# Kernel tuning notes

Measured on AMD Instinct MI355X. Metric: run time of the kernel, lower is better.

Reference implementation:

```python
import jax, jax.numpy as jnp
import numpy as np
import math

B, S, D, NH, HFF, E, K, C, L, V = 8, 256, 1024, 16, 2048, 8, 2, 10, 4, 32000
HD = D // NH
EPS = 1e-5


def _pos_encoding(max_len, d_model):
    pos = jnp.arange(max_len, dtype=jnp.float32)[:, None]
    div = jnp.exp(jnp.arange(0, d_model, 2, dtype=jnp.float32) * (-math.log(10000.0) / d_model))
    pe = jnp.zeros((max_len, d_model), dtype=jnp.float32)
    pe = pe.at[:, 0::2].set(jnp.sin(pos * div))
    pe = pe.at[:, 1::2].set(jnp.cos(pos * div))
    return pe[:, None, :]  # [max_len, 1, D], matching torch buffer layout


def _layernorm(x, g, b):
    mu = jnp.mean(x, axis=-1, keepdims=True)
    var = jnp.mean((x - mu) ** 2, axis=-1, keepdims=True)
    return (x - mu) * jax.lax.rsqrt(var + EPS) * g + b


def setup_inputs() -> dict:
    key = jax.random.key(0)
    ks = jax.random.split(key, 20)
    sc = lambda *shape: 0.02
    inp = {
        "src": jax.random.randint(ks[0], (B, S), 0, V, dtype=jnp.int32),
        "emb": jax.random.normal(ks[1], (V, D), jnp.float32) * 0.02,
        "in_proj_w": jax.random.normal(ks[2], (L, 3 * D, D), jnp.float32) * 0.02,
        "in_proj_b": jnp.zeros((L, 3 * D), jnp.float32),
        "out_w": jax.random.normal(ks[3], (L, D, D), jnp.float32) * 0.02,
        "out_b": jnp.zeros((L, D), jnp.float32),
        "ln1_g": jnp.ones((L, D), jnp.float32),
        "ln1_b": jnp.zeros((L, D), jnp.float32),
        "ln2_g": jnp.ones((L, D), jnp.float32),
        "ln2_b": jnp.zeros((L, D), jnp.float32),
        "gate_w": jax.random.normal(ks[4], (L, E, D), jnp.float32) * 0.02,
        "gate_b": jnp.zeros((L, E), jnp.float32),
        "w1": jax.random.normal(ks[5], (L, E, D, HFF), jnp.float32) * 0.02,
        "b1": jnp.zeros((L, E, HFF), jnp.float32),
        "w2": jax.random.normal(ks[6], (L, E, HFF, D), jnp.float32) * 0.02,
        "b2": jnp.zeros((L, E, D), jnp.float32),
        "cls_w": jax.random.normal(ks[7], (C, D), jnp.float32) * 0.02,
        "cls_b": jnp.zeros((C,), jnp.float32),
    }
    return inp


def _attention(x, ipw, ipb, ow, ob):
    # x: [B,S,D]
    qkv = x @ ipw.T + ipb  # [B,S,3D]
    q, k, v = jnp.split(qkv, 3, axis=-1)
    q = q.reshape(B, S, NH, HD)
    k = k.reshape(B, S, NH, HD)
    v = v.reshape(B, S, NH, HD)
    scores = jnp.einsum("bqhd,bkhd->bhqk", q, k) / math.sqrt(HD)
    attn = jax.nn.softmax(scores, axis=-1)
    o = jnp.einsum("bhqk,bkhd->bqhd", attn, v).reshape(B, S, D)
    return o @ ow.T + ob


def _moe(x, gw, gb, w1, b1, w2, b2):
    # x: [B,S,D]; gw: [E,D]; w1: [E,D,H]; w2: [E,H,D]
    t = x.reshape(B * S, D)
    logits = t @ gw.T + gb  # [T,E]
    topv, topi = jax.lax.top_k(logits, K)  # [T,K]
    weights = jax.nn.softmax(topv, axis=-1)  # [T,K]
    # dense expert compute (small E, compute-bound), combine via top-k gather
    h = jax.nn.relu(jnp.einsum("td,edh->teh", t, w1) + b1)  # [T,E,H]
    y = jnp.einsum("teh,ehd->ted", h, w2) + b2  # [T,E,D]
    sel = jnp.take_along_axis(y, topi[:, :, None], axis=1)  # [T,K,D]
    out = jnp.sum(sel * weights[:, :, None], axis=1)  # [T,D]
    return out.reshape(B, S, D), logits.reshape(B, S, E)


def reference(src, emb, in_proj_w, in_proj_b, out_w, out_b, ln1_g, ln1_b,
              ln2_g, ln2_b, gate_w, gate_b, w1, b1, w2, b2, cls_w, cls_b):
    x = emb[src] * math.sqrt(D)  # [B,S,D]
    pe = _pos_encoding(5000, D)  # [max_len,1,D]
    # faithful to original: pe indexed by batch dim (x.size(0)), broadcast over seq
    x = x + pe[:B]  # [B,1,D] -> broadcast [B,S,D]
    all_gates = []
    for l in range(in_proj_w.shape[0]):
        a = _attention(x, in_proj_w[l], in_proj_b[l], out_w[l], out_b[l])
        x = _layernorm(x + a, ln1_g[l], ln1_b[l])
        m, g = _moe(x, gate_w[l], gate_b[l], w1[l], b1[l], w2[l], b2[l])
        x = _layernorm(x + m, ln2_g[l], ln2_b[l])
        all_gates.append(g)
    pooled = jnp.mean(x, axis=1)  # [B,D]
    out = pooled @ cls_w.T + cls_b  # [B,C]
    return out, jnp.stack(all_gates)  # ([B,C], [L,B,S,E])
```

## Files before the change

### kernel.cpp

```cpp
#include <hip/hip_runtime.h>
#include <math.h>

#define TKN 2048
#define DIM 1024
#define NHEAD 16
#define HDIM 64
#define HFF 2048
#define NE 8
#define TOPK 2
#define NCLS 10
#define NLAYER 4
#define SEQ 256
#define BATCH 8

typedef __attribute__((ext_vector_type(8))) _Float16 f16x8;
typedef __attribute__((ext_vector_type(4))) float f32x4;

__device__ __forceinline__ unsigned short f2h(float v) {
  _Float16 h = (_Float16)v;
  return __builtin_bit_cast(unsigned short, h);
}
__device__ __forceinline__ float h2f(unsigned short u) {
  return (float)__builtin_bit_cast(_Float16, u);
}
__device__ __forceinline__ void fsplit(float v, unsigned short& hi, unsigned short& lo) {
  _Float16 h = (_Float16)v;
  hi = __builtin_bit_cast(unsigned short, h);
  lo = f2h(v - (float)h);
}

__device__ __forceinline__ void gload_lds16(const void* g, void* l) {
  __builtin_amdgcn_global_load_lds((__attribute__((address_space(1))) void*)g,
                                   (__attribute__((address_space(3))) void*)l,
                                   16, 0, 0);
}

__global__ __launch_bounds__(256) void k_embed(const int* __restrict__ src,
                                               const float* __restrict__ emb,
                                               float* __restrict__ x,
                                               unsigned short* __restrict__ xhi,
                                               unsigned short* __restrict__ xlo) {
  const int t = blockIdx.x;
  const int tid = threadIdx.x;
  const int b = t / SEQ;
  const int tok = src[t];
  const float* erow = emb + (size_t)tok * DIM;
  const size_t base = (size_t)t * DIM;
  const float cexp = -9.210340371976184f / 1024.0f;
#pragma unroll
  for (int j = 0; j < 4; ++j) {
    int d = tid + 256 * j;
    int i2 = d & ~1;
    float ang = (float)b * expf((float)i2 * cexp);
    float pe = (d & 1) ? cosf(ang) : sinf(ang);
    float v = erow[d] * 32.0f + pe;
    x[base + d] = v;
    fsplit(v, xhi[base + d], xlo[base + d]);
  }
}

__global__ __launch_bounds__(256) void k_cvt_split(const float* __restrict__ in,
                                                   unsigned short* __restrict__ ohi,
                                                   unsigned short* __restrict__ olo) {
  int i = blockIdx.x * 256 + threadIdx.x;
  float4 v = ((const float4*)in)[i];
  ushort4 h, l;
  fsplit(v.x, h.x, l.x); fsplit(v.y, h.y, l.y);
  fsplit(v.z, h.z, l.z); fsplit(v.w, h.w, l.w);
  ((ushort4*)ohi)[i] = h;
  ((ushort4*)olo)[i] = l;
}

__global__ __launch_bounds__(256) void k_cvt_t_split(const float* __restrict__ in,
                                                     unsigned short* __restrict__ ohi,
                                                     unsigned short* __restrict__ olo,
                                                     int R, int Cc) {
  __shared__ float t[32][33];
  const int tx = threadIdx.x & 31, ty = threadIdx.x >> 5;
  const int c0 = blockIdx.x * 32, r0 = blockIdx.y * 32;
  const float* ip = in + (size_t)blockIdx.z * R * Cc;
  const size_t obase = (size_t)blockIdx.z * R * Cc;
#pragma unroll
  for (int j = 0; j < 4; ++j)
    t[ty + 8 * j][tx] = ip[(size_t)(r0 + ty + 8 * j) * Cc + c0 + tx];
  __syncthreads();
#pragma unroll
  for (int j = 0; j < 4; ++j) {
    unsigned short hi, lo;
    fsplit(t[tx][ty + 8 * j], hi, lo);
    size_t o = obase + (size_t)(c0 + ty + 8 * j) * R + r0 + tx;
    ohi[o] = hi;
    olo[o] = lo;
  }
}

template <int MODE, bool RELU, int OUTK, bool SPLIT>
__global__ __launch_bounds__(256) void k_mfma_gemm(
    const unsigned short* __restrict__ Ahi, const unsigned short* __restrict__ Alo,
    const unsigned short* __restrict__ Bhi, const unsigned short* __restrict__ Blo,
    const float* __restrict__ bias, void* __restrict__ out0, void* __restrict__ out1,
    int M, int N, int K,
    const int* __restrict__ slot_token, const int* __restrict__ offg) {
  __shared__ unsigned short U[SPLIT ? 2 : 1][128 * 64];
  const int tid = threadIdx.x;
  const int w = tid >> 6, lane = tid & 63;
  const int bm = blockIdx.y * 128, bn = blockIdx.x * 128;
  int r0 = 0, rows = M, e = 0;
  if (MODE != 0) {
    e = blockIdx.z;
    r0 = offg[e];
    rows = offg[e + 1] - r0;
    if (bm >= rows) return;
  }
  const size_t bwb = (size_t)e * K * N;
  const float* biasq = bias + (size_t)e * N;

  const int lrow8 = lane >> 3;
  const int s = (lane & 7) ^ lrow8;
  const int chunk = (s & 3) * 8;
  const unsigned short* sp0[4];
  const unsigned short* sp1[4];
#pragma unroll
  for (int i = 0; i < 4; ++i) {
    int rloc = w * 32 + i * 8 + lrow8;
    int growA;
    if (MODE == 0) {
      growA = bm + rloc;
    } else {
      int rr = bm + rloc;
      if (rr >= rows) rr = rows - 1;
      growA = (MODE == 1) ? slot_token[r0 + rr] : (r0 + rr);
    }
    size_t aoff = (size_t)growA * K + chunk;
    size_t boff = bwb + (size_t)(bn + rloc) * K + chunk;
    if constexpr (SPLIT) {
      sp0[i] = (s < 4 ? Ahi : Alo) + aoff;
      sp1[i] = (s < 4 ? Bhi : Blo) + boff;
    } else {
      sp0[i] = (s < 4) ? (Ahi + aoff) : (Bhi + boff);
      sp1[i] = nullptr;
    }
  }

  f32x4 acc[4][4] = {};
  const int wr = w >> 1, wc = w & 1;
  const int lr = lane & 15, lg = lane >> 4;
  const int sw = lr & 7;
  unsigned aoffs[4], boffs[4];
#pragma unroll
  for (int m = 0; m < 4; ++m)
    aoffs[m] = (unsigned)((wr * 64 + m * 16 + lr) * 64 + ((lg ^ sw) * 8));
#pragma unroll
  for (int n = 0; n < 4; ++n)
    boffs[n] = (unsigned)((wc * 64 + n * 16 + lr) * 64 + ((lg ^ sw) * 8));

  for (int k0 = 0; k0 < K; k0 += 32) {
#pragma unroll
    for (int i = 0; i < 4; ++i) {
      gload_lds16(sp0[i], &U[0][(w * 32 + i * 8) * 64]);
      sp0[i] += 32;
      if constexpr (SPLIT) {
        gload_lds16(sp1[i], &U[1][(w * 32 + i * 8) * 64]);
        sp1[i] += 32;
      }
    }
    __syncthreads();
    f16x8 afh[4], bfh[4], afl[4], bfl[4];
    if constexpr (SPLIT) {
#pragma unroll
      for (int m = 0; m < 4; ++m) afh[m] = *(const f16x8*)&U[0][aoffs[m]];
#pragma unroll
      for (int m = 0; m < 4; ++m) afl[m] = *(const f16x8*)&U[0][aoffs[m] ^ 32];
#pragma unroll
      for (int n = 0; n < 4; ++n) bfh[n] = *(const f16x8*)&U[1][boffs[n]];
#pragma unroll
      for (int n = 0; n < 4; ++n) bfl[n] = *(const f16x8*)&U[1][boffs[n] ^ 32];
    } else {
#pragma unroll
      for (int m = 0; m < 4; ++m) afh[m] = *(const f16x8*)&U[0][aoffs[m]];
#pragma unroll
      for (int n = 0; n < 4; ++n) bfh[n] = *(const f16x8*)&U[0][boffs[n] ^ 32];
    }
#pragma unroll
    for (int m = 0; m < 4; ++m)
#pragma unroll
      for (int n = 0; n < 4; ++n) {
        acc[m][n] = __builtin_amdgcn_mfma_f32_16x16x32_f16(afh[m], bfh[n], acc[m][n], 0, 0, 0);
        if constexpr (SPLIT) {
          acc[m][n] = __builtin_amdgcn_mfma_f32_16x16x32_f16(afh[m], bfl[n], acc[m][n], 0, 0, 0);
          acc[m][n] = __builtin_amdgcn_mfma_f32_16x16x32_f16(afl[m], bfh[n], acc[m][n], 0, 0, 0);
        }
      }
    __syncthreads();
  }

  float bv[4];
#pragma unroll
  for (int n = 0; n < 4; ++n) bv[n] = biasq[bn + wc * 64 + n * 16 + lr];

#pragma unroll
  for (int m = 0; m < 4; ++m) {
#pragma unroll
    for (int j = 0; j < 4; ++j) {
      int rowg = bm + wr * 64 + m * 16 + lg * 4 + j;
      if (MODE != 0 && rowg >= rows) continue;
      size_t crow = (size_t)((MODE == 0) ? rowg : (r0 + rowg)) * N;
#pragma unroll
      for (int n = 0; n < 4; ++n) {
        float v = acc[m][n][j] + bv[n];
        if (RELU) v = fmaxf(v, 0.f);
        size_t o = crow + bn + wc * 64 + n * 16 + lr;
        if (OUTK == 0) {
          ((float*)out0)[o] = v;
        } else if (OUTK == 1) {
          ((unsigned short*)out0)[o] = f2h(v);
        } else {
          unsigned short hi, lo;
          fsplit(v, hi, lo);
          ((unsigned short*)out0)[o] = hi;
          ((unsigned short*)out1)[o] = lo;
        }
      }
    }
  }
}

__global__ __launch_bounds__(256) void k_attn(const float* __restrict__ qkv,
                                              unsigned short* __restrict__ ohi,
                                              unsigned short* __restrict__ olo) {
  const int qt = blockIdx.x;
  const int hh = blockIdx.y;
  const int bb = blockIdx.z;
  const int tid = threadIdx.x;
  __shared__ float qs[16][64];
  __shared__ float ps[16][256];
  const int t0 = bb * SEQ + qt * 16;
  for (int i = tid; i < 16 * 64; i += 256) {
    int qi = i >> 6, d = i & 63;
    qs[qi][d] = qkv[(size_t)(t0 + qi) * (3 * DIM) + hh * 64 + d];
  }
  __syncthreads();
  float s[16];
#pragma unroll
  for (int qi = 0; qi < 16; ++qi) s[qi] = 0.f;
  const float* krow = qkv + (size_t)(bb * SEQ + tid) * (3 * DIM) + DIM + hh * 64;
#pragma unroll 4
  for (int c = 0; c < 16; ++c) {
    float4 kv = *(const float4*)(krow + c * 4);
#pragma unroll
    for (int qi = 0; qi < 16; ++qi) {
      s[qi] += kv.x * qs[qi][c * 4 + 0] + kv.y * qs[qi][c * 4 + 1] +
               kv.z * qs[qi][c * 4 + 2] + kv.w * qs[qi][c * 4 + 3];
    }
  }
#pragma unroll
  for (int qi = 0; qi < 16; ++qi) ps[qi][tid] = s[qi] * 0.125f;
  __syncthreads();
  const int wv = tid >> 6, lane = tid & 63;
  for (int rr = wv; rr < 16; rr += 4) {
    float v[4];
#pragma unroll
    for (int j = 0; j < 4; ++j) v[j] = ps[rr][lane + 64 * j];
    float m = fmaxf(fmaxf(v[0], v[1]), fmaxf(v[2], v[3]));
    for (int msk = 32; msk; msk >>= 1) m = fmaxf(m, __shfl_xor(m, msk));
    float e[4], sum = 0.f;
#pragma unroll
    for (int j = 0; j < 4; ++j) { e[j] = expf(v[j] - m); sum += e[j]; }
    for (int msk = 32; msk; msk >>= 1) sum += __shfl_xor(sum, msk);
    float inv = 1.0f / sum;
#pragma unroll
    for (int j = 0; j < 4; ++j) ps[rr][lane + 64 * j] = e[j] * inv;
  }
  __syncthreads();
  const int qi0 = tid >> 6, d = tid & 63;
  float acc[4] = {0.f, 0.f, 0.f, 0.f};
  const float* vbase = qkv + (size_t)(bb * SEQ) * (3 * DIM) + 2 * DIM + hh * 64 + d;
  for (int k = 0; k < 256; ++k) {
    float vv = vbase[(size_t)k * (3 * DIM)];
    acc[0] += ps[qi0][k] * vv;
    acc[1] += ps[qi0 + 4][k] * vv;
    acc[2] += ps[qi0 + 8][k] * vv;
    acc[3] += ps[qi0 + 12][k] * vv;
  }
#pragma unroll
  for (int j = 0; j < 4; ++j) {
    size_t o = (size_t)(t0 + qi0 + 4 * j) * DIM + hh * 64 + d;
    fsplit(acc[j], ohi[o], olo[o]);
  }
}

__device__ __forceinline__ float block_reduce_sum(float v, float* red) {
  const int tid = threadIdx.x;
  red[tid] = v;
  __syncthreads();
  for (int s = 128; s > 0; s >>= 1) {
    if (tid < s) red[tid] += red[tid + s];
    __syncthreads();
  }
  float r = red[0];
  __syncthreads();
  return r;
}

__global__ __launch_bounds__(256) void k_add_ln(const float* __restrict__ xin,
                                                const float* __restrict__ add,
                                                const float* __restrict__ g,
                                                const float* __restrict__ bt,
                                                float* __restrict__ xout,
                                                unsigned short* __restrict__ xhi,
                                                unsigned short* __restrict__ xlo) {
  __shared__ float red[256];
  const int t = blockIdx.x, tid = threadIdx.x;
  const size_t base = (size_t)t * DIM;
  float v[4];
  float s = 0.f;
#pragma unroll
  for (int j = 0; j < 4; ++j) {
    int d = tid + 256 * j;
    v[j] = xin[base + d] + add[base + d];
    s += v[j];
  }
  float mean = block_reduce_sum(s, red) * (1.0f / DIM);
  float s2 = 0.f;
#pragma unroll
  for (int j = 0; j < 4; ++j) { float dv = v[j] - mean; s2 += dv * dv; }
  float var = block_reduce_sum(s2, red) * (1.0f / DIM);
  float rs = rsqrtf(var + 1e-5f);
#pragma unroll
  for (int j = 0; j < 4; ++j) {
    int d = tid + 256 * j;
    float o = (v[j] - mean) * rs * g[d] + bt[d];
    xout[base + d] = o;
    fsplit(o, xhi[base + d], xlo[base + d]);
  }
}

__global__ __launch_bounds__(256) void k_gate(const float* __restrict__ x,
                                              const float* __restrict__ gw,
                                              const float* __restrict__ gb,
                                              float* __restrict__ gout,
                                              int* __restrict__ topi,
                                              float* __restrict__ topw) {
  __shared__ float xs[DIM];
  __shared__ float lgs[NE];
  const int t = blockIdx.x, tid = threadIdx.x;
#pragma unroll
  for (int j = 0; j < 4; ++j) xs[tid + 256 * j] = x[(size_t)t * DIM + tid + 256 * j];
  __syncthreads();
  const int eg = tid >> 5, l32 = tid & 31;
  const float* wrow = gw + (size_t)eg * DIM;
  float p = 0.f;
  for (int j = 0; j < 32; ++j) {
    int d = l32 + 32 * j;
    p += xs[d] * wrow[d];
  }
  for (int m = 16; m; m >>= 1) p += __shfl_xor(p, m);
  if (l32 == 0) lgs[eg] = p;
  __syncthreads();
  if (tid < NE) {
    float v = lgs[tid] + gb[tid];
    gout[(size_t)t * NE + tid] = v;
    lgs[tid] = v;
  }
  __syncthreads();
  if (tid == 0) {
    int i0 = 0; float v0 = lgs[0];
    for (int i = 1; i < NE; ++i) if (lgs[i] > v0) { v0 = lgs[i]; i0 = i; }
    int i1 = -1; float v1 = -1e30f;
    for (int i = 0; i < NE; ++i) { if (i == i0) continue; if (lgs[i] > v1) { v1 = lgs[i]; i1 = i; } }
    float e1 = expf(v1 - v0);
    float w0 = 1.0f / (1.0f + e1);
    topi[2 * t] = i0; topi[2 * t + 1] = i1;
    topw[2 * t] = w0; topw[2 * t + 1] = e1 * w0;
  }
}

__global__ __launch_bounds__(512) void k_route(const int* __restrict__ topi,
                                               int* __restrict__ offg,
                                               int* __restrict__ slot_token,
                                               int* __restrict__ slot_of) {
  __shared__ int cnt_s[NE];
  __shared__ int off_s[NE + 1];
  const int tid = threadIdx.x;
  const int w = tid >> 6, lane = tid & 63;
  int c = 0;
  for (int i = lane; i < TKN * TOPK; i += 64) c += (topi[i] == w) ? 1 : 0;
  for (int m = 32; m; m >>= 1) c += __shfl_xor(c, m);
  if (lane == 0) cnt_s[w] = c;
  __syncthreads();
  if (tid == 0) {
    off_s[0] = 0;
    for (int e2 = 0; e2 < NE; ++e2) off_s[e2 + 1] = off_s[e2] + cnt_s[e2];
    for (int e2 = 0; e2 <= NE; ++e2) offg[e2] = off_s[e2];
  }
  __syncthreads();
  int base = off_s[w];
  for (int i0 = 0; i0 < TKN * TOPK; i0 += 64) {
    int i = i0 + lane;
    bool mm = (topi[i] == w);
    unsigned long long mask = __ballot(mm ? 1 : 0);
    int rank = __popcll(mask & ((1ull << lane) - 1ull));
    if (mm) {
      int slot = base + rank;
      slot_token[slot] = i >> 1;
      slot_of[i] = slot;
    }
    base += __popcll(mask);
  }
}

__global__ __launch_bounds__(256) void k_moe_combine_ln(const float* __restrict__ xin,
                                                        const float* __restrict__ y,
                                                        const float* __restrict__ topw,
                                                        const int* __restrict__ slot_of,
                                                        const float* __restrict__ g,
                                                        const float* __restrict__ bt,
                                                        float* __restrict__ xout,
                                                        unsigned short* __restrict__ xhi,
                                                        unsigned short* __restrict__ xlo) {
  __shared__ float red[256];
  const int t = blockIdx.x, tid = threadIdx.x;
  const float w0 = topw[2 * t], w1v = topw[2 * t + 1];
  const int s0 = slot_of[2 * t], s1 = slot_of[2 * t + 1];
  const size_t base = (size_t)t * DIM;
  float v[4];
  float s = 0.f;
#pragma unroll
  for (int j = 0; j < 4; ++j) {
    int d = tid + 256 * j;
    v[j] = xin[base + d] + w0 * y[(size_t)s0 * DIM + d] + w1v * y[(size_t)s1 * DIM + d];
    s += v[j];
  }
  float mean = block_reduce_sum(s, red) * (1.0f / DIM);
  float s2 = 0.f;
#pragma unroll
  for (int j = 0; j < 4; ++j) { float dv = v[j] - mean; s2 += dv * dv; }
  float var = block_reduce_sum(s2, red) * (1.0f / DIM);
  float rs = rsqrtf(var + 1e-5f);
#pragma unroll
  for (int j = 0; j < 4; ++j) {
    int d = tid + 256 * j;
    float o = (v[j] - mean) * rs * g[d] + bt[d];
    xout[base + d] = o;
    fsplit(o, xhi[base + d], xlo[base + d]);
  }
}

__global__ __launch_bounds__(256) void k_pool_cls(const float* __restrict__ x,
                                                  const float* __restrict__ cw,
                                                  const float* __restrict__ cb,
                                                  float* __restrict__ out) {
  __shared__ float pooled[DIM];
  const int b = blockIdx.x, tid = threadIdx.x;
  float a[4] = {0.f, 0.f, 0.f, 0.f};
  for (int s = 0; s < SEQ; ++s) {
    const float* row = x + (size_t)(b * SEQ + s) * DIM;
#pragma unroll
    for (int j = 0; j < 4; ++j) a[j] += row[tid + 256 * j];
  }
#pragma unroll
  for (int j = 0; j < 4; ++j) pooled[tid + 256 * j] = a[j] * (1.0f / SEQ);
  __syncthreads();
  const int wv = tid >> 6, lane = tid & 63;
  for (int c = wv; c < NCLS; c += 4) {
    float p = 0.f;
    for (int d = lane; d < DIM; d += 64) p += pooled[d] * cw[(size_t)c * DIM + d];
    for (int m = 32; m; m >>= 1) p += __shfl_xor(p, m);
    if (lane == 0) out[b * NCLS + c] = p + cb[c];
  }
}

extern "C" void kernel_launch(void* const* d_in, const int* in_sizes, int n_in,
                              void* d_out, int out_size, void* d_ws, size_t ws_size,
                              hipStream_t stream) {
  const int*   src  = (const int*)  d_in[0];
  const float* emb  = (const float*)d_in[1];
  const float* ipw  = (const float*)d_in[2];
  const float* ipb  = (const float*)d_in[3];
  const float* ow   = (const float*)d_in[4];
  const float* ob   = (const float*)d_in[5];
  const float* ln1g = (const float*)d_in[6];
  const float* ln1b = (const float*)d_in[7];
  const float* ln2g = (const float*)d_in[8];
  const float* ln2b = (const float*)d_in[9];
  const float* gw   = (const float*)d_in[10];
  const float* gb   = (const float*)d_in[11];
  const float* w1   = (const float*)d_in[12];
  const float* b1   = (const float*)d_in[13];
  const float* w2   = (const float*)d_in[14];
  const float* b2   = (const float*)d_in[15];
  const float* cw   = (const float*)d_in[16];
  const float* cb   = (const float*)d_in[17];
  float* out = (float*)d_out;

  char* ws = (char*)d_ws;
  size_t off = 0;
  auto carve = [&](size_t bytes) -> void* {
    void* p = ws + off;
    off += (bytes + 255) & ~(size_t)255;
    return p;
  };
  float*          x     = (float*)carve((size_t)TKN * DIM * 4);
  unsigned short* xhi   = (unsigned short*)carve((size_t)TKN * DIM * 2);
  unsigned short* xlo   = (unsigned short*)carve((size_t)TKN * DIM * 2);
  char*           bufQ  = (char*)carve((size_t)2 * TKN * TOPK * HFF * 2);
  float*          qkv   = (float*)bufQ;
  unsigned short* h_hi  = (unsigned short*)bufQ;
  unsigned short* h_lo  = (unsigned short*)(bufQ + (size_t)TKN * TOPK * HFF * 2);
  unsigned short* at_hi = (unsigned short*)carve((size_t)TKN * DIM * 2);
  unsigned short* at_lo = (unsigned short*)carve((size_t)TKN * DIM * 2);
  char*           bufP  = (char*)carve((size_t)TKN * TOPK * DIM * 4);
  float*          proj  = (float*)bufP;
  float*          ybuf  = (float*)bufP;
  unsigned short* wq_hi = (unsigned short*)carve((size_t)3 * DIM * DIM * 2);
  unsigned short* wq_lo = (unsigned short*)carve((size_t)3 * DIM * DIM * 2);
  unsigned short* wo_hi = (unsigned short*)carve((size_t)DIM * DIM * 2);
  unsigned short* wo_lo = (unsigned short*)carve((size_t)DIM * DIM * 2);
  unsigned short* wt_hi = (unsigned short*)carve((size_t)NE * DIM * HFF * 2);
  unsigned short* wt_lo = (unsigned short*)carve((size_t)NE * DIM * HFF * 2);
  float* topw       = (float*)carve((size_t)TKN * TOPK * 4);
  int*   topi       = (int*)  carve((size_t)TKN * TOPK * 4);
  int*   slot_token = (int*)  carve((size_t)TKN * TOPK * 4);
  int*   slot_of    = (int*)  carve((size_t)TKN * TOPK * 4);
  int*   offg       = (int*)  carve(64);

  k_embed<<<TKN, 256, 0, stream>>>(src, emb, x, xhi, xlo);

  for (int l = 0; l < NLAYER; ++l) {
    const float* ipw_l = ipw + (size_t)l * 3 * DIM * DIM;
    const float* ow_l  = ow  + (size_t)l * DIM * DIM;
    const float* w1_l  = w1  + (size_t)l * NE * DIM * HFF;
    const float* w2_l  = w2  + (size_t)l * NE * HFF * DIM;
    const bool sp = (l < NLAYER - 1);

    k_cvt_split<<<(3 * DIM * DIM) / 1024, 256, 0, stream>>>(ipw_l, wq_hi, wq_lo);
    k_cvt_split<<<(DIM * DIM) / 1024, 256, 0, stream>>>(ow_l, wo_hi, wo_lo);
    k_cvt_t_split<<<dim3(HFF / 32, DIM / 32, NE), 256, 0, stream>>>(w1_l, wt_hi, wt_lo, DIM, HFF);

    if (sp)
      k_mfma_gemm<0, false, 0, true><<<dim3(3 * DIM / 128, TKN / 128), 256, 0, stream>>>(
          xhi, xlo, wq_hi, wq_lo, ipb + (size_t)l * 3 * DIM, qkv, nullptr, TKN, 3 * DIM, DIM, nullptr, nullptr);
    else
      k_mfma_gemm<0, false, 0, false><<<dim3(3 * DIM / 128, TKN / 128), 256, 0, stream>>>(
          xhi, xlo, wq_hi, wq_lo, ipb + (size_t)l * 3 * DIM, qkv, nullptr, TKN, 3 * DIM, DIM, nullptr, nullptr);

    k_attn<<<dim3(SEQ / 16, NHEAD, BATCH), 256, 0, stream>>>(qkv, at_hi, at_lo);

    if (sp)
      k_mfma_gemm<0, false, 0, true><<<dim3(DIM / 128, TKN / 128), 256, 0, stream>>>(
          at_hi, at_lo, wo_hi, wo_lo, ob + (size_t)l * DIM, proj, nullptr, TKN, DIM, DIM, nullptr, nullptr);
    else
      k_mfma_gemm<0, false, 0, false><<<dim3(DIM / 128, TKN / 128), 256, 0, stream>>>(
          at_hi, at_lo, wo_hi, wo_lo, ob + (size_t)l * DIM, proj, nullptr, TKN, DIM, DIM, nullptr, nullptr);

    k_add_ln<<<TKN, 256, 0, stream>>>(x, proj, ln1g + l * DIM, ln1b + l * DIM, x, xhi, xlo);

    k_gate<<<TKN, 256, 0, stream>>>(x, gw + (size_t)l * NE * DIM, gb + l * NE,
                                    out + NCLS * BATCH + (size_t)l * TKN * NE, topi, topw);
    k_route<<<1, 512, 0, stream>>>(topi, offg, slot_token, slot_of);

    if (sp)
      k_mfma_gemm<1, true, 2, true><<<dim3(HFF / 128, TKN * TOPK / 128, NE), 256, 0, stream>>>(
          xhi, xlo, wt_hi, wt_lo, b1 + (size_t)l * NE * HFF, h_hi, h_lo, 0, HFF, DIM, slot_token, offg);
    else
      k_mfma_gemm<1, true, 1, false><<<dim3(HFF / 128, TKN * TOPK / 128, NE), 256, 0, stream>>>(
          xhi, xlo, wt_hi, wt_lo, b1 + (size_t)l * NE * HFF, h_hi, nullptr, 0, HFF, DIM, slot_token, offg);

    k_cvt_t_split<<<dim3(DIM / 32, HFF / 32, NE), 256, 0, stream>>>(w2_l, wt_hi, wt_lo, HFF, DIM);

    if (sp)
      k_mfma_gemm<2, false, 0, true><<<dim3(DIM / 128, TKN * TOPK / 128, NE), 256, 0, stream>>>(
          h_hi, h_lo, wt_hi, wt_lo, b2 + (size_t)l * NE * DIM, ybuf, nullptr, 0, DIM, HFF, nullptr, offg);
    else
      k_mfma_gemm<2, false, 0, false><<<dim3(DIM / 128, TKN * TOPK / 128, NE), 256, 0, stream>>>(
          h_hi, h_lo, wt_hi, wt_lo, b2 + (size_t)l * NE * DIM, ybuf, nullptr, 0, DIM, HFF, nullptr, offg);

    k_moe_combine_ln<<<TKN, 256, 0, stream>>>(x, ybuf, topw, slot_of,
                                              ln2g + l * DIM, ln2b + l * DIM, x, xhi, xlo);
  }
  k_pool_cls<<<BATCH, 256, 0, stream>>>(x, cw, cb, out);
}
```

Measured before the change: 1.741 ms.

## Double-buffer LDS tiles in MFMA GEMM to overlap global loads with compute

The shared-memory tile becomes a ping-pong buffer. The next K-slice's global-to-LDS loads are issued before the MFMA work on the current slice, so memory latency can hide behind compute. The previous load, barrier, compute, barrier loop becomes one wait plus barrier per iteration. This doubles LDS use (64KB for the split variant), which may reduce occupancy. Correctness relies on the explicit vmcnt wait ordering the direct-to-LDS loads.

```diff
diff --git a/kernel.cpp b/kernel.cpp
--- a/kernel.cpp
+++ b/kernel.cpp
@@ -101,7 +101,8 @@
     const float* __restrict__ bias, void* __restrict__ out0, void* __restrict__ out1,
     int M, int N, int K,
     const int* __restrict__ slot_token, const int* __restrict__ offg) {
-  __shared__ unsigned short U[SPLIT ? 2 : 1][128 * 64];
+  constexpr int NP = SPLIT ? 2 : 1;
+  __shared__ unsigned short U[2][NP][128 * 64];
   const int tid = threadIdx.x;
   const int w = tid >> 6, lane = tid & 63;
   const int bm = blockIdx.y * 128, bn = blockIdx.x * 128;
@@ -154,32 +155,48 @@
   for (int n = 0; n < 4; ++n)
     boffs[n] = (unsigned)((wc * 64 + n * 16 + lr) * 64 + ((lg ^ sw) * 8));
 
-  for (int k0 = 0; k0 < K; k0 += 32) {
-#pragma unroll
-    for (int i = 0; i < 4; ++i) {
-      gload_lds16(sp0[i], &U[0][(w * 32 + i * 8) * 64]);
-      sp0[i] += 32;
-      if constexpr (SPLIT) {
-        gload_lds16(sp1[i], &U[1][(w * 32 + i * 8) * 64]);
-        sp1[i] += 32;
+#pragma unroll
+  for (int i = 0; i < 4; ++i) {
+    gload_lds16(sp0[i], &U[0][0][(w * 32 + i * 8) * 64]);
+    sp0[i] += 32;
+    if constexpr (SPLIT) {
+      gload_lds16(sp1[i], &U[0][1][(w * 32 + i * 8) * 64]);
+      sp1[i] += 32;
+    }
+  }
+  asm volatile("s_waitcnt vmcnt(0)" ::: "memory");
+  __builtin_amdgcn_s_barrier();
+
+  const int NT = K / 32;
+#pragma unroll 2
+  for (int t = 0; t < NT; ++t) {
+    const int cur = t & 1;
+    if (t + 1 < NT) {
+#pragma unroll
+      for (int i = 0; i < 4; ++i) {
+        gload_lds16(sp0[i], &U[cur ^ 1][0][(w * 32 + i * 8) * 64]);
+        sp0[i] += 32;
+        if constexpr (SPLIT) {
+          gload_lds16(sp1[i], &U[cur ^ 1][1][(w * 32 + i * 8) * 64]);
+          sp1[i] += 32;
+        }
       }
     }
-    __syncthreads();
     f16x8 afh[4], bfh[4], afl[4], bfl[4];
     if constexpr (SPLIT) {
 #pragma unroll
-      for (int m = 0; m < 4; ++m) afh[m] = *(const f16x8*)&U[0][aoffs[m]];
-#pragma unroll
-      for (int m = 0; m < 4; ++m) afl[m] = *(const f16x8*)&U[0][aoffs[m] ^ 32];
-#pragma unroll
-      for (int n = 0; n < 4; ++n) bfh[n] = *(const f16x8*)&U[1][boffs[n]];
-#pragma unroll
-      for (int n = 0; n < 4; ++n) bfl[n] = *(const f16x8*)&U[1][boffs[n] ^ 32];
+      for (int m = 0; m < 4; ++m) afh[m] = *(const f16x8*)&U[cur][0][aoffs[m]];
+#pragma unroll
+      for (int m = 0; m < 4; ++m) afl[m] = *(const f16x8*)&U[cur][0][aoffs[m] ^ 32];
+#pragma unroll
+      for (int n = 0; n < 4; ++n) bfh[n] = *(const f16x8*)&U[cur][1][boffs[n]];
+#pragma unroll
+      for (int n = 0; n < 4; ++n) bfl[n] = *(const f16x8*)&U[cur][1][boffs[n] ^ 32];
     } else {
 #pragma unroll
-      for (int m = 0; m < 4; ++m) afh[m] = *(const f16x8*)&U[0][aoffs[m]];
-#pragma unroll
-      for (int n = 0; n < 4; ++n) bfh[n] = *(const f16x8*)&U[0][boffs[n] ^ 32];
+      for (int m = 0; m < 4; ++m) afh[m] = *(const f16x8*)&U[cur][0][aoffs[m]];
+#pragma unroll
+      for (int n = 0; n < 4; ++n) bfh[n] = *(const f16x8*)&U[cur][0][boffs[n] ^ 32];
     }
 #pragma unroll
     for (int m = 0; m < 4; ++m)
@@ -191,7 +208,8 @@
           acc[m][n] = __builtin_amdgcn_mfma_f32_16x16x32_f16(afl[m], bfh[n], acc[m][n], 0, 0, 0);
         }
       }
-    __syncthreads();
+    asm volatile("s_waitcnt vmcnt(0)" ::: "memory");
+    __builtin_amdgcn_s_barrier();
   }
 
   float bv[4];
```

After: 1.568 ms. 1.11x faster.
